# Performance work log

Measured on AMD Instinct MI355X. Metric: run time of the kernel, lower is better.

Reference implementation:

```python
import jax, jax.numpy as jnp
import numpy as np

EMBED_DIM = 1024
NUM_HEADS = 16
HEAD_DIM = EMBED_DIM // NUM_HEADS  # 64
BATCH = 4
SEQ_LEN = 2048
TOTAL = BATCH * SEQ_LEN
SOFTMAX_SCALE = 1.0 / np.sqrt(64.0)  # hard-coded 1/sqrt(64) in the source


def setup_inputs() -> dict:
    key = jax.random.key(0)
    ks = jax.random.split(key, 5)
    hidden_states = jax.random.normal(ks[0], (TOTAL, EMBED_DIM), jnp.float32)
    proj_weight = jax.random.normal(ks[1], (3 * EMBED_DIM, EMBED_DIM), jnp.float32) * 0.02
    proj_bias = jax.random.normal(ks[2], (3 * EMBED_DIM,), jnp.float32) * 0.02
    out_weight = jax.random.normal(ks[3], (EMBED_DIM, EMBED_DIM), jnp.float32) * 0.02
    out_bias = jax.random.normal(ks[4], (EMBED_DIM,), jnp.float32) * 0.02
    cu_seqlens = jnp.arange(BATCH + 1, dtype=jnp.int32) * SEQ_LEN
    return {
        "hidden_states": hidden_states,
        "proj_weight": proj_weight,
        "proj_bias": proj_bias,
        "out_weight": out_weight,
        "out_bias": out_bias,
        "cu_seqlens": cu_seqlens,
        "max_len": SEQ_LEN,
    }


def reference(hidden_states, proj_weight, proj_bias, out_weight, out_bias, cu_seqlens, max_len):
    # fused QKV projection: [T, 3E]
    T = hidden_states.shape[0]
    B = cu_seqlens.shape[0] - 1  # static; equal-length packed sequences
    S = T // B
    qkv = hidden_states @ proj_weight.T + proj_bias
    # per-head interleaved layout, matching qkv.view(T, H, 3, D)
    qkv = qkv.reshape(B, S, NUM_HEADS, 3, HEAD_DIM)
    q = qkv[..., 0, :]  # [B, S, H, D]
    k = qkv[..., 1, :]
    v = qkv[..., 2, :]
    scores = jnp.einsum("bqhd,bkhd->bhqk", q, k) * SOFTMAX_SCALE
    attn = jax.nn.softmax(scores, axis=-1)  # non-causal (is_decoder=False)
    ctx = jnp.einsum("bhqk,bkhd->bqhd", attn, v)
    ctx = ctx.reshape(T, NUM_HEADS * HEAD_DIM)
    out = ctx @ out_weight.T + out_bias
    return out
```

## Files before the change

### kernel.cpp

```cpp
#include <hip/hip_runtime.h>
#include <stdint.h>
#include <math.h>
#include <type_traits>


typedef float f32x4 __attribute__((ext_vector_type(4)));
typedef __bf16 bf16x8 __attribute__((ext_vector_type(8)));
typedef __bf16 bf16x4 __attribute__((ext_vector_type(4)));
typedef unsigned short u16x4 __attribute__((ext_vector_type(4)));

#define EMB 1024
#define SEQ 2048
#define NBH 64
#define QSCALE 0.1803368801111204f

__device__ __forceinline__ unsigned short f2bf(float f) {
  unsigned int u = __builtin_bit_cast(unsigned int, f);
  u += 0x7FFFu + ((u >> 16) & 1u);
  return (unsigned short)(u >> 16);
}

__device__ __forceinline__ float fast_exp2(float x) {
  float r;
  asm("v_exp_f32 %0, %1" : "=v"(r) : "v"(x));
  return r;
}

__device__ __forceinline__ void gl_lds16(const void* g, void* l) {
  __builtin_amdgcn_global_load_lds(
      (const __attribute__((address_space(1))) unsigned int*)g,
      (__attribute__((address_space(3))) unsigned int*)l, 16, 0, 0);
}

#define N1 2097152u
#define N2 786432u
#define N3 262144u

__global__ __launch_bounds__(256) void convert_k(
    const float* __restrict__ hs, const float* __restrict__ wq,
    const float* __restrict__ wo, unsigned short* __restrict__ hb,
    unsigned short* __restrict__ wqb, unsigned short* __restrict__ wob) {
  unsigned int i = blockIdx.x * 256u + threadIdx.x;
  const float* src; unsigned short* dst; unsigned int off;
  if (i < N1)            { src = hs; dst = hb;  off = i; }
  else if (i < N1 + N2)  { src = wq; dst = wqb; off = i - N1; }
  else                   { src = wo; dst = wob; off = i - (N1 + N2); }
  float4 v = ((const float4*)src)[off];
  u16x4 o;
  o[0] = f2bf(v.x); o[1] = f2bf(v.y); o[2] = f2bf(v.z); o[3] = f2bf(v.w);
  ((u16x4*)dst)[off] = o;
}

template <int EPI>
__global__ __launch_bounds__(256) void gemm_bt(
    const __bf16* __restrict__ A, const __bf16* __restrict__ B,
    const float* __restrict__ bias, float* __restrict__ outF,
    unsigned short* __restrict__ Qg, unsigned short* __restrict__ Kg,
    unsigned short* __restrict__ Vt) {
  __shared__ __bf16 As[128 * 64];
  __shared__ __bf16 Bs[128 * 64];
  const int tid = threadIdx.x;
  const int lane = tid & 63, w = tid >> 6;
  const int wm = w >> 1, wn = w & 1;
  const int l15 = lane & 15, g = lane >> 4;
  const int m0 = blockIdx.y * 128;
  const int n0 = blockIdx.x * 128;

  f32x4 acc[4][4] = {};

  for (int kt = 0; kt < 16; ++kt) {
    const int k0 = kt * 64;
#pragma unroll
    for (int i = 0; i < 4; ++i) {
      int p = i * 256 + tid;
      int row = p >> 3, cp = p & 7;
      int c = cp ^ (row & 7);
      gl_lds16(A + (size_t)(m0 + row) * 1024 + k0 + c * 8, (char*)As + p * 16);
      gl_lds16(B + (size_t)(n0 + row) * 1024 + k0 + c * 8, (char*)Bs + p * 16);
    }
    __syncthreads();
#pragma unroll
    for (int kc = 0; kc < 2; ++kc) {
      bf16x8 af[4], bfr[4];
#pragma unroll
      for (int mf = 0; mf < 4; ++mf) {
        int row = wm * 64 + mf * 16 + l15;
        int c = (kc * 4 + g) ^ (row & 7);
        af[mf] = *(const bf16x8*)((const char*)As + row * 128 + c * 16);
      }
#pragma unroll
      for (int nf = 0; nf < 4; ++nf) {
        int row = wn * 64 + nf * 16 + l15;
        int c = (kc * 4 + g) ^ (row & 7);
        bfr[nf] = *(const bf16x8*)((const char*)Bs + row * 128 + c * 16);
      }
#pragma unroll
      for (int mf = 0; mf < 4; ++mf)
#pragma unroll
        for (int nf = 0; nf < 4; ++nf)
          acc[mf][nf] = __builtin_amdgcn_mfma_f32_16x16x32_bf16(
              af[mf], bfr[nf], acc[mf][nf], 0, 0, 0);
    }
    __syncthreads();
  }

  if (EPI == 0) {
#pragma unroll
    for (int nf = 0; nf < 4; ++nf) {
      int colb = n0 + wn * 64 + nf * 16;
      int h = colb / 192;
      int rb = colb - h * 192;
      int which = rb >> 6;
      int d = (rb & 63) + l15;
      float bv = bias[colb + l15];
#pragma unroll
      for (int mf = 0; mf < 4; ++mf) {
        int t0 = m0 + wm * 64 + mf * 16 + g * 4;
        int b = t0 >> 11, s0 = t0 & 2047;
        size_t bhb = (size_t)(b * 16 + h) * 131072;
        if (which == 2) {
          u16x4 pk;
#pragma unroll
          for (int j = 0; j < 4; ++j) pk[j] = f2bf(acc[mf][nf][j] + bv);
          *(u16x4*)(Vt + bhb + (size_t)d * 2048 + s0) = pk;
        } else {
          unsigned short* dst = (which == 0) ? Qg : Kg;
          float sc = (which == 0) ? QSCALE : 1.0f;
#pragma unroll
          for (int j = 0; j < 4; ++j)
            dst[bhb + (size_t)(s0 + j) * 64 + d] = f2bf((acc[mf][nf][j] + bv) * sc);
        }
      }
    }
  } else {
#pragma unroll
    for (int nf = 0; nf < 4; ++nf) {
      int col = n0 + wn * 64 + nf * 16 + l15;
      float bv = bias[col];
#pragma unroll
      for (int mf = 0; mf < 4; ++mf) {
        int r0 = m0 + wm * 64 + mf * 16 + g * 4;
#pragma unroll
        for (int j = 0; j < 4; ++j)
          outF[(size_t)(r0 + j) * 1024 + col] = acc[mf][nf][j] + bv;
      }
    }
  }
}

__global__ __launch_bounds__(256) void attn_k(
    const __bf16* __restrict__ Qg, const __bf16* __restrict__ Kg,
    const __bf16* __restrict__ Vt, unsigned short* __restrict__ ctxg) {
  __shared__ __bf16 Ks[2][64 * 64];
  __shared__ __bf16 Vs[2][64 * 64];
  __shared__ __bf16 Ps[4][32 * 64];
  const int tid = threadIdx.x;
  const int lane = tid & 63, w = tid >> 6;
  const int l15 = lane & 15, g = lane >> 4;
  const int bid = blockIdx.x;
  const int wg = (bid & 7) * 128 + (bid >> 3);
  const int bh = wg >> 4;
  const int qt = wg & 15;
  const size_t base = (size_t)bh * 131072;
  const int qbase = qt * 128 + w * 32;

  const int sp0 = tid, sp1 = 256 + tid;
  const int srow0 = sp0 >> 3, sw0 = (sp0 & 7) ^ (srow0 & 7);
  const int srow1 = sp1 >> 3, sw1 = (sp1 & 7) ^ (srow1 & 7);

  bf16x8 qf[2][2];
#pragma unroll
  for (int qs = 0; qs < 2; ++qs)
#pragma unroll
    for (int kc = 0; kc < 2; ++kc)
      qf[qs][kc] = *(const bf16x8*)(Qg + base + (size_t)(qbase + qs * 16 + l15) * 64 +
                                    kc * 32 + g * 8);

  bf16x8 ones;
#pragma unroll
  for (int i = 0; i < 8; ++i) ones[i] = (__bf16)1.0f;

  f32x4 ctx[2][4] = {};
  f32x4 ctx_sum[2] = {};
  char* const pbase_w = (char*)&Ps[w][0];

  gl_lds16(Kg + base + (size_t)srow0 * 64 + sw0 * 8, (char*)&Ks[0][0] + sp0 * 16);
  gl_lds16(Vt + base + (size_t)srow0 * 2048 + sw0 * 8, (char*)&Vs[0][0] + sp0 * 16);
  gl_lds16(Kg + base + (size_t)srow1 * 64 + sw1 * 8, (char*)&Ks[0][0] + sp1 * 16);
  gl_lds16(Vt + base + (size_t)srow1 * 2048 + sw1 * 8, (char*)&Vs[0][0] + sp1 * 16);
  __syncthreads();

  auto tile_pass = [&](auto CURC, int kb, bool stage_next) {
    constexpr int CUR = decltype(CURC)::value;
    const char* const kbuf = (const char*)&Ks[CUR][0];
    const char* const vbuf = (const char*)&Vs[CUR][0];

    if (stage_next) {
      const int nkb = kb + 64;
      char* const nk = (char*)&Ks[CUR ^ 1][0];
      char* const nv = (char*)&Vs[CUR ^ 1][0];
      gl_lds16(Kg + base + (size_t)(nkb + srow0) * 64 + sw0 * 8, nk + sp0 * 16);
      gl_lds16(Vt + base + (size_t)srow0 * 2048 + nkb + sw0 * 8, nv + sp0 * 16);
      gl_lds16(Kg + base + (size_t)(nkb + srow1) * 64 + sw1 * 8, nk + sp1 * 16);
      gl_lds16(Vt + base + (size_t)srow1 * 2048 + nkb + sw1 * 8, nv + sp1 * 16);
    }

    f32x4 sc[4][2];
#pragma unroll
    for (int kt4 = 0; kt4 < 4; ++kt4) {
      int krow = kt4 * 16 + l15;
      bf16x8 kf0 = *(const bf16x8*)(kbuf + krow * 128 + ((g ^ (krow & 7)) * 16));
      bf16x8 kf1 = *(const bf16x8*)(kbuf + krow * 128 + (((4 + g) ^ (krow & 7)) * 16));
#pragma unroll
      for (int qs = 0; qs < 2; ++qs) {
        f32x4 a = {0.f, 0.f, 0.f, 0.f};
        a = __builtin_amdgcn_mfma_f32_16x16x32_bf16(kf0, qf[qs][0], a, 0, 0, 0);
        a = __builtin_amdgcn_mfma_f32_16x16x32_bf16(kf1, qf[qs][1], a, 0, 0, 0);
        sc[kt4][qs] = a;
      }
    }

#pragma unroll
    for (int qs = 0; qs < 2; ++qs) {
      int q = qs * 16 + l15;
      char* pb = pbase_w + q * 128;
#pragma unroll
      for (int kt4 = 0; kt4 < 4; ++kt4) {
        int k0 = kt4 * 16 + g * 4;
        bf16x4 pk = {(__bf16)fast_exp2(sc[kt4][qs][0]),
                     (__bf16)fast_exp2(sc[kt4][qs][1]),
                     (__bf16)fast_exp2(sc[kt4][qs][2]),
                     (__bf16)fast_exp2(sc[kt4][qs][3])};
        *(bf16x4*)(pb + (((k0 >> 3) ^ (q & 7)) * 16) + (k0 & 7) * 2) = pk;
      }
    }

    asm volatile("" ::: "memory");

#pragma unroll
    for (int kc = 0; kc < 2; ++kc) {
      bf16x8 pfr[2], vfr[4];
#pragma unroll
      for (int qs = 0; qs < 2; ++qs) {
        int q = qs * 16 + l15;
        int c = (kc * 4 + g) ^ (q & 7);
        pfr[qs] = *(const bf16x8*)(pbase_w + q * 128 + c * 16);
      }
#pragma unroll
      for (int ds = 0; ds < 4; ++ds) {
        int row = ds * 16 + l15;
        int c = (kc * 4 + g) ^ (row & 7);
        vfr[ds] = *(const bf16x8*)(vbuf + row * 128 + c * 16);
      }
#pragma unroll
      for (int qs = 0; qs < 2; ++qs) {
#pragma unroll
        for (int ds = 0; ds < 4; ++ds)
          ctx[qs][ds] = __builtin_amdgcn_mfma_f32_16x16x32_bf16(
              pfr[qs], vfr[ds], ctx[qs][ds], 0, 0, 0);
        ctx_sum[qs] = __builtin_amdgcn_mfma_f32_16x16x32_bf16(
            pfr[qs], ones, ctx_sum[qs], 0, 0, 0);
      }
    }

    __syncthreads();
  };

  for (int t = 0; t < 32; t += 2) {
    tile_pass(std::integral_constant<int, 0>{}, t * 64, true);
    tile_pass(std::integral_constant<int, 1>{}, (t + 1) * 64, t + 2 < 32);
  }

  const int b = bh >> 4, h = bh & 15;
#pragma unroll
  for (int qs = 0; qs < 2; ++qs) {
#pragma unroll
    for (int j = 0; j < 4; ++j) {
      float inv = 1.0f / ctx_sum[qs][j];
      int q = qbase + qs * 16 + g * 4 + j;
      size_t trow = (size_t)(b * 2048 + q) * 1024 + h * 64;
#pragma unroll
      for (int ds = 0; ds < 4; ++ds) {
        __bf16 ov = (__bf16)(ctx[qs][ds][j] * inv);
        ctxg[trow + ds * 16 + l15] = __builtin_bit_cast(unsigned short, ov);
      }
    }
  }
}

extern "C" void kernel_launch(void* const* d_in, const int* in_sizes, int n_in,
                              void* d_out, int out_size, void* d_ws, size_t ws_size,
                              hipStream_t stream) {
  (void)in_sizes; (void)n_in; (void)out_size; (void)ws_size;
  const float* hs   = (const float*)d_in[0];
  const float* wqkv = (const float*)d_in[1];
  const float* bqkv = (const float*)d_in[2];
  const float* wout = (const float*)d_in[3];
  const float* bout = (const float*)d_in[4];

  char* ws = (char*)d_ws;
  unsigned short* hb  = (unsigned short*)(ws + 0);
  unsigned short* ctx = (unsigned short*)(ws + 0);
  unsigned short* wqb = (unsigned short*)(ws + 16777216);
  unsigned short* wob = (unsigned short*)(ws + 23068672);
  unsigned short* Qg  = (unsigned short*)(ws + 25165824);
  unsigned short* Kg  = (unsigned short*)(ws + 41943040);
  unsigned short* Vt  = (unsigned short*)(ws + 58720256);

  hipLaunchKernelGGL(convert_k, dim3(12288), dim3(256), 0, stream,
                     hs, wqkv, wout, hb, wqb, wob);
  hipLaunchKernelGGL((gemm_bt<0>), dim3(24, 64), dim3(256), 0, stream,
                     (const __bf16*)hb, (const __bf16*)wqb, bqkv, (float*)nullptr,
                     Qg, Kg, Vt);
  hipLaunchKernelGGL(attn_k, dim3(1024), dim3(256), 0, stream,
                     (const __bf16*)Qg, (const __bf16*)Kg, (const __bf16*)Vt, ctx);
  hipLaunchKernelGGL((gemm_bt<1>), dim3(8, 64), dim3(256), 0, stream,
                     (const __bf16*)ctx, (const __bf16*)wob, bout, (float*)d_out,
                     (unsigned short*)nullptr, (unsigned short*)nullptr,
                     (unsigned short*)nullptr);
}
```

Before: 193.3 us.

## Remap GEMM blocks per XCD and stage V-transpose stores through LDS

Both GEMMs now launch on a 1D grid and remap block ids so each group of eight consecutive ids is spread across chiplets, keeping neighbouring tiles on the same XCD for L2 reuse. The QKV epilogue stages the V tile through per-wave LDS scratch so each lane writes two 16-byte contiguous chunks of the transposed V instead of scattered 8-byte stores. The LDS reuse relies on the final syncthreads of the main loop, and the swizzle assumes the block count divides evenly by eight.

```diff
diff --git a/kernel.cpp b/kernel.cpp
--- a/kernel.cpp
+++ b/kernel.cpp
@@ -8,6 +8,7 @@
 typedef __bf16 bf16x8 __attribute__((ext_vector_type(8)));
 typedef __bf16 bf16x4 __attribute__((ext_vector_type(4)));
 typedef unsigned short u16x4 __attribute__((ext_vector_type(4)));
+typedef unsigned int u32x4 __attribute__((ext_vector_type(4)));
 
 #define EMB 1024
 #define SEQ 2048
@@ -63,8 +64,12 @@
   const int lane = tid & 63, w = tid >> 6;
   const int wm = w >> 1, wn = w & 1;
   const int l15 = lane & 15, g = lane >> 4;
-  const int m0 = blockIdx.y * 128;
-  const int n0 = blockIdx.x * 128;
+  constexpr int NX = (EPI == 0) ? 24 : 8;
+  constexpr int NB = (EPI == 0) ? 1536 : 512;
+  const int bid = blockIdx.x;
+  const int swz = (bid & 7) * (NB / 8) + (bid >> 3);
+  const int m0 = (swz / NX) * 128;
+  const int n0 = (swz % NX) * 128;
 
   f32x4 acc[4][4] = {};
 
@@ -105,6 +110,10 @@
   }
 
   if (EPI == 0) {
+    char* const scr = (char*)As + w * 4096;
+    const int t0base = m0 + wm * 64;
+    const int bb = t0base >> 11, s0base = t0base & 2047;
+    (void)bb;
 #pragma unroll
     for (int nf = 0; nf < 4; ++nf) {
       int colb = n0 + wn * 64 + nf * 16;
@@ -113,19 +122,28 @@
       int which = rb >> 6;
       int d = (rb & 63) + l15;
       float bv = bias[colb + l15];
-#pragma unroll
-      for (int mf = 0; mf < 4; ++mf) {
-        int t0 = m0 + wm * 64 + mf * 16 + g * 4;
-        int b = t0 >> 11, s0 = t0 & 2047;
-        size_t bhb = (size_t)(b * 16 + h) * 131072;
-        if (which == 2) {
+      size_t bhb = (size_t)((t0base >> 11) * 16 + h) * 131072;
+      if (which == 2) {
+#pragma unroll
+        for (int mf = 0; mf < 4; ++mf) {
           u16x4 pk;
 #pragma unroll
           for (int j = 0; j < 4; ++j) pk[j] = f2bf(acc[mf][nf][j] + bv);
-          *(u16x4*)(Vt + bhb + (size_t)d * 2048 + s0) = pk;
-        } else {
-          unsigned short* dst = (which == 0) ? Qg : Kg;
-          float sc = (which == 0) ? QSCALE : 1.0f;
+          *(u16x4*)(scr + l15 * 144 + (mf * 16 + g * 4) * 2) = pk;
+        }
+        asm volatile("" ::: "memory");
+        u32x4 lo = *(const u32x4*)(scr + l15 * 144 + g * 32);
+        u32x4 hi = *(const u32x4*)(scr + l15 * 144 + g * 32 + 16);
+        asm volatile("" ::: "memory");
+        unsigned short* vdst = Vt + bhb + (size_t)d * 2048 + s0base + g * 16;
+        *(u32x4*)(vdst) = lo;
+        *(u32x4*)(vdst + 8) = hi;
+      } else {
+        unsigned short* dst = (which == 0) ? Qg : Kg;
+        float sc = (which == 0) ? QSCALE : 1.0f;
+#pragma unroll
+        for (int mf = 0; mf < 4; ++mf) {
+          int s0 = s0base + mf * 16 + g * 4;
 #pragma unroll
           for (int j = 0; j < 4; ++j)
             dst[bhb + (size_t)(s0 + j) * 64 + d] = f2bf((acc[mf][nf][j] + bv) * sc);
@@ -309,12 +327,12 @@
 
   hipLaunchKernelGGL(convert_k, dim3(12288), dim3(256), 0, stream,
                      hs, wqkv, wout, hb, wqb, wob);
-  hipLaunchKernelGGL((gemm_bt<0>), dim3(24, 64), dim3(256), 0, stream,
+  hipLaunchKernelGGL((gemm_bt<0>), dim3(1536), dim3(256), 0, stream,
                      (const __bf16*)hb, (const __bf16*)wqb, bqkv, (float*)nullptr,
                      Qg, Kg, Vt);
   hipLaunchKernelGGL(attn_k, dim3(1024), dim3(256), 0, stream,
                      (const __bf16*)Qg, (const __bf16*)Kg, (const __bf16*)Vt, ctx);
-  hipLaunchKernelGGL((gemm_bt<1>), dim3(8, 64), dim3(256), 0, stream,
+  hipLaunchKernelGGL((gemm_bt<1>), dim3(512), dim3(256), 0, stream,
                      (const __bf16*)ctx, (const __bf16*)wob, bout, (float*)d_out,
                      (unsigned short*)nullptr, (unsigned short*)nullptr,
                      (unsigned short*)nullptr);
```

After: 192.3 us. Within noise of the previous version (-0.5%).
